# Performance work log

Measured on AMD Instinct MI355X. Metric: run time of the kernel, lower is better.

The kernel has to match this reference:

```python
import jax, jax.numpy as jnp
import numpy as np

HEADS = 4
DIM_HEAD = 64
SCALE = DIM_HEAD ** -0.5


def setup_inputs() -> dict:
    key = jax.random.key(0)
    k1, k2, k3 = jax.random.split(key, 3)
    C = 256
    hidden = HEADS * DIM_HEAD  # 256
    x = jax.random.normal(k1, (16, C, 64, 64), dtype=jnp.float32)
    # 1x1 conv weights collapsed to [out, in] matrices
    w_qkv = jax.random.normal(k2, (3 * hidden, C), dtype=jnp.float32) * (C ** -0.5)
    w_out = jax.random.normal(k3, (C, hidden), dtype=jnp.float32) * (hidden ** -0.5)
    b_out = jnp.zeros((C,), dtype=jnp.float32)
    return {"x": x, "w_qkv": w_qkv, "w_out": w_out, "b_out": b_out}


def reference(x, w_qkv, w_out, b_out):
    b, c, h, w = x.shape
    n = h * w
    # 1x1 conv == channel GEMM
    qkv = jnp.einsum('bchw,oc->bohw', x, w_qkv)           # [b, 3*hidden, h, w]
    qkv = qkv.reshape(b, 3, HEADS, DIM_HEAD, n)            # [b, 3, H, d, n]
    q, k, v = qkv[:, 0], qkv[:, 1], qkv[:, 2]              # each [b, H, d, n]
    q = jax.nn.softmax(q, axis=2) * SCALE                  # softmax over d
    k = jax.nn.softmax(k, axis=3)                          # softmax over n
    context = jnp.einsum('bhdn,bhen->bhde', k, v)          # [b, H, d, e]
    out = jnp.einsum('bhde,bhdn->bhen', context, q)        # [b, H, e, n]
    out = out.reshape(b, HEADS * DIM_HEAD, h, w)           # [b, hidden, h, w]
    return jnp.einsum('bchw,oc->bohw', out, w_out) + b_out[None, :, None, None]
```

## Files before the change

kernel.cpp:

```cpp
#include <hip/hip_runtime.h>

#define NPIX 4096
#define SCALE 0.125f

typedef _Float16 half8 __attribute__((ext_vector_type(8)));
typedef _Float16 half4 __attribute__((ext_vector_type(4)));
typedef float floatx4 __attribute__((ext_vector_type(4)));

__device__ __forceinline__ void async16(void* lds, const void* g) {
  __builtin_amdgcn_global_load_lds(
      (const __attribute__((address_space(1))) unsigned int*)(uintptr_t)g,
      (__attribute__((address_space(3))) unsigned int*)(unsigned)(uintptr_t)lds,
      16, 0, 0);
}

__global__ __launch_bounds__(256) void split16_kernel(const float* __restrict__ w,
                                                      _Float16* __restrict__ hi,
                                                      _Float16* __restrict__ lo, int n) {
  int i = blockIdx.x * 256 + threadIdx.x;
  if (i < n) {
    float v = w[i];
    _Float16 h = (_Float16)v;
    hi[i] = h;
    lo[i] = (_Float16)(v - (float)h);
  }
}

__global__ __launch_bounds__(256) void transpose16_kernel(const float* __restrict__ x,
                                                          _Float16* __restrict__ xt) {
  __shared__ float t[64][65];
  const int n0 = blockIdx.x * 64, c0 = blockIdx.y * 64, b = blockIdx.z;
  const float* xp = x + (long)b * 256 * NPIX;
  const int tid = threadIdx.x;
  const int r = tid >> 4, c4 = (tid & 15) * 4;
#pragma unroll
  for (int p = 0; p < 4; p++) {
    float4 v = *(const float4*)&xp[(long)(c0 + r + p * 16) * NPIX + n0 + c4];
    t[r + p * 16][c4 + 0] = v.x;
    t[r + p * 16][c4 + 1] = v.y;
    t[r + p * 16][c4 + 2] = v.z;
    t[r + p * 16][c4 + 3] = v.w;
  }
  __syncthreads();
  const int n = tid >> 2, cg = (tid & 3) * 16;
  alignas(16) _Float16 o[16];
#pragma unroll
  for (int i = 0; i < 16; i++) o[i] = (_Float16)t[cg + i][n];
  _Float16* dst = &xt[((long)b * NPIX + n0 + n) * 256 + c0 + cg];
  *(float4*)dst = *(float4*)&o[0];
  *(float4*)(dst + 8) = *(float4*)&o[8];
}

__global__ __launch_bounds__(256) void q_gemm_softmax(const _Float16* __restrict__ Ahp,
                                                      const _Float16* __restrict__ Alp,
                                                      const _Float16* __restrict__ Bt,
                                                      _Float16* __restrict__ PT) {
  union alignas(16) QU {
    _Float16 st[2][3][128 * 32];
    _Float16 pt[128][128];
  };
  __shared__ QU u;
  const int tid = threadIdx.x;
  const int n0 = blockIdx.x * 128, m0 = blockIdx.y * 128;
  const int bz = blockIdx.z;
  const _Float16* Bp = Bt + (long)bz * NPIX * 256;
  const int wv = tid >> 6, l = tid & 63;
  const int r16 = l & 15, q = l >> 4;
  const int mb = (wv >> 1) * 64, nb = (wv & 1) * 64;
  const int r1 = tid >> 2;
  const int o1 = ((tid & 3) * 8) ^ (((r1 >> 1) & 3) * 8);
  const int r2 = r1 + 64;
  const int ldsc1 = (wv * 64) * 8;
  const int ldsc2 = (256 + wv * 64) * 8;
  const int q8 = (q * 8) ^ (((r16 >> 1) & 3) * 8);

  auto STAGE = [&](int buf, int kt) {
    const int k0 = kt * 32;
    async16(&u.st[buf][0][ldsc1], &Ahp[(long)(m0 + r1) * 256 + k0 + o1]);
    async16(&u.st[buf][0][ldsc2], &Ahp[(long)(m0 + r2) * 256 + k0 + o1]);
    async16(&u.st[buf][1][ldsc1], &Alp[(long)(m0 + r1) * 256 + k0 + o1]);
    async16(&u.st[buf][1][ldsc2], &Alp[(long)(m0 + r2) * 256 + k0 + o1]);
    async16(&u.st[buf][2][ldsc1], &Bp[(long)(n0 + r1) * 256 + k0 + o1]);
    async16(&u.st[buf][2][ldsc2], &Bp[(long)(n0 + r2) * 256 + k0 + o1]);
  };

  floatx4 acc[4][4];
#pragma unroll
  for (int i = 0; i < 4; i++)
#pragma unroll
    for (int j = 0; j < 4; j++) acc[i][j] = (floatx4){0.f, 0.f, 0.f, 0.f};

  STAGE(0, 0);
  __syncthreads();
  int cur = 0;
  for (int kt = 0; kt < 8; kt++) {
    if (kt < 7) STAGE(cur ^ 1, kt + 1);
    half8 fa[4], flo[4], fb[4];
#pragma unroll
    for (int i = 0; i < 4; i++) {
      fa[i] = *(const half8*)&u.st[cur][0][(mb + i * 16 + r16) * 32 + q8];
      flo[i] = *(const half8*)&u.st[cur][1][(mb + i * 16 + r16) * 32 + q8];
      fb[i] = *(const half8*)&u.st[cur][2][(nb + i * 16 + r16) * 32 + q8];
    }
#pragma unroll
    for (int i = 0; i < 4; i++)
#pragma unroll
      for (int j = 0; j < 4; j++) {
        acc[i][j] = __builtin_amdgcn_mfma_f32_16x16x32_f16(fa[i], fb[j], acc[i][j], 0, 0, 0);
        acc[i][j] = __builtin_amdgcn_mfma_f32_16x16x32_f16(flo[i], fb[j], acc[i][j], 0, 0, 0);
      }
    __syncthreads();
    cur ^= 1;
  }

#pragma unroll
  for (int j = 0; j < 4; j++) {
    float s = 0.f;
#pragma unroll
    for (int i = 0; i < 4; i++)
#pragma unroll
      for (int t = 0; t < 4; t++) {
        float e = __expf(acc[i][j][t]);
        acc[i][j][t] = e;
        s += e;
      }
    s += __shfl_xor(s, 16, 64);
    s += __shfl_xor(s, 32, 64);
    const float rinv = 1.0f / s;
    const int nl = nb + j * 16 + r16;
    const int swz = (nl & 7) * 8;
#pragma unroll
    for (int i = 0; i < 4; i++) {
      half4 h4;
#pragma unroll
      for (int t = 0; t < 4; t++) h4[t] = (_Float16)(acc[i][j][t] * rinv);
      *(half4*)&u.pt[nl][(mb + i * 16 + q * 4) ^ swz] = h4;
    }
  }
  __syncthreads();
  const int rbase = tid >> 4, c16 = tid & 15;
  _Float16* dst = PT + ((long)(bz * 2 + (m0 >> 7)) * NPIX + n0) * 128;
#pragma unroll
  for (int k = 0; k < 8; k++) {
    const int row = rbase + k * 16;
    const int chunk = c16 ^ (row & 7);
    float4 v = *(const float4*)&u.pt[row][chunk * 8];
    *(float4*)&dst[(long)row * 128 + c16 * 8] = v;
  }
}

#define CPB 2
__global__ __launch_bounds__(256) void kv_ctx_gemm(const _Float16* __restrict__ Ahp,
                                                   const _Float16* __restrict__ Bt,
                                                   float* __restrict__ pbuf,
                                                   float* __restrict__ rsbuf) {
  union alignas(16) KVU {
    _Float16 st[2][2][128 * 32];
    _Float16 ev[128][136];
  };
  __shared__ KVU u;
  const int tid = threadIdx.x;
  const int cg = blockIdx.x;
  const int hi = blockIdx.y;
  const int b = blockIdx.z;
  const _Float16* Bp = Bt + (long)b * NPIX * 256;
  const int wv = tid >> 6, l = tid & 63;
  const int r16 = l & 15, q = l >> 4;
  const int mb = (wv >> 1) * 64, nb = (wv & 1) * 64;
  const int r1 = tid >> 2;
  const int o1 = ((tid & 3) * 8) ^ (((r1 >> 1) & 3) * 8);
  const int ldsc1 = (wv * 64) * 8;
  const int ldsc2 = (256 + wv * 64) * 8;
  const int q8 = (q * 8) ^ (((r16 >> 1) & 3) * 8);
  const long gAk = (long)(256 + hi * 64 + r1) * 256;
  const long gAv = (long)(512 + hi * 64 + r1) * 256;

  auto STAGE = [&](int buf, int kt, int n0) {
    const int k0 = kt * 32;
    async16(&u.st[buf][0][ldsc1], &Ahp[gAk + k0 + o1]);
    async16(&u.st[buf][0][ldsc2], &Ahp[gAv + k0 + o1]);
    async16(&u.st[buf][1][ldsc1], &Bp[(long)(n0 + r1) * 256 + k0 + o1]);
    async16(&u.st[buf][1][ldsc2], &Bp[(long)(n0 + 64 + r1) * 256 + k0 + o1]);
  };

  floatx4 c2[4];
#pragma unroll
  for (int j = 0; j < 4; j++) c2[j] = (floatx4){0.f, 0.f, 0.f, 0.f};
  float rs = 0.f;

  for (int cs = 0; cs < CPB; cs++) {
    const int n0 = (cg * CPB + cs) * 128;
    floatx4 acc[4][4];
#pragma unroll
    for (int i = 0; i < 4; i++)
#pragma unroll
      for (int j = 0; j < 4; j++) acc[i][j] = (floatx4){0.f, 0.f, 0.f, 0.f};

    STAGE(0, 0, n0);
    __syncthreads();
    int cur = 0;
    for (int kt = 0; kt < 8; kt++) {
      if (kt < 7) STAGE(cur ^ 1, kt + 1, n0);
      half8 fa[4], fb[4];
#pragma unroll
      for (int i = 0; i < 4; i++) {
        fa[i] = *(const half8*)&u.st[cur][0][(mb + i * 16 + r16) * 32 + q8];
        fb[i] = *(const half8*)&u.st[cur][1][(nb + i * 16 + r16) * 32 + q8];
      }
#pragma unroll
      for (int i = 0; i < 4; i++)
#pragma unroll
        for (int j = 0; j < 4; j++) {
          acc[i][j] = __builtin_amdgcn_mfma_f32_16x16x32_f16(fa[i], fb[j], acc[i][j], 0, 0, 0);
        }
      __syncthreads();
      cur ^= 1;
    }

    const bool is_k = (mb == 0);
#pragma unroll
    for (int i = 0; i < 4; i++) {
      const int row = mb + i * 16 + q * 4;
#pragma unroll
      for (int j = 0; j < 4; j++) {
        const int col = nb + j * 16 + r16;
#pragma unroll
        for (int t = 0; t < 4; t++) {
          const float vv0 = acc[i][j][t];
          u.ev[row + t][col] = (_Float16)(is_k ? __expf(vv0) : vv0);
        }
      }
    }
    __syncthreads();

#pragma unroll
    for (int ks = 0; ks < 4; ks++) {
      half8 a = *(const half8*)&u.ev[wv * 16 + r16][ks * 32 + q * 8];
#pragma unroll
      for (int ii = 0; ii < 8; ii++) rs += (float)a[ii];
#pragma unroll
      for (int j = 0; j < 4; j++) {
        half8 bv = *(const half8*)&u.ev[64 + j * 16 + r16][ks * 32 + q * 8];
        c2[j] = __builtin_amdgcn_mfma_f32_16x16x32_f16(a, bv, c2[j], 0, 0, 0);
      }
    }
    __syncthreads();
  }

  rs += __shfl_xor(rs, 16, 64);
  rs += __shfl_xor(rs, 32, 64);
  const int bh = b * 4 + hi;
  float* pp = pbuf + ((long)bh * 16 + cg) * 4096;
#pragma unroll
  for (int j = 0; j < 4; j++)
#pragma unroll
    for (int reg = 0; reg < 4; reg++)
      pp[(wv * 16 + q * 4 + reg) * 64 + j * 16 + r16] = c2[j][reg];
  if (l < 16) rsbuf[((long)bh * 16 + cg) * 64 + wv * 16 + r16] = rs;
}

__global__ __launch_bounds__(256) void mctx_fused(const float* __restrict__ w_out,
                                                  const float* __restrict__ pbuf,
                                                  const float* __restrict__ rsbuf,
                                                  _Float16* __restrict__ Mhi,
                                                  _Float16* __restrict__ Mlo) {
  __shared__ float sctxT[64][65];
  __shared__ float sinv[64];
  const int cq = blockIdx.x, h = blockIdx.y, b = blockIdx.z;
  const int bh = b * 4 + h;
  const float* pp = pbuf + (long)bh * 16 * 4096;
  const int tid = threadIdx.x;
  {
    const int d = tid >> 2, e0 = (tid & 3) * 16;
    float s0[16];
#pragma unroll
    for (int i = 0; i < 16; i++) s0[i] = 0.f;
    for (int c = 0; c < 16; c++) {
#pragma unroll
      for (int k = 0; k < 4; k++) {
        float4 v = *(const float4*)&pp[(long)c * 4096 + d * 64 + e0 + k * 4];
        s0[k * 4 + 0] += v.x;
        s0[k * 4 + 1] += v.y;
        s0[k * 4 + 2] += v.z;
        s0[k * 4 + 3] += v.w;
      }
    }
#pragma unroll
    for (int i = 0; i < 16; i++) sctxT[e0 + i][d] = s0[i];
  }
  if (tid < 64) {
    const float* rp = rsbuf + (long)bh * 16 * 64 + tid;
    float z = 0.f;
#pragma unroll
    for (int c = 0; c < 16; c++) z += rp[c * 64];
    sinv[tid] = 1.0f / z;
  }
  __syncthreads();
  const int c = cq * 64 + (tid >> 2);
  const int d0 = (tid & 3) * 16;
  const float* wp = w_out + (long)c * 256 + h * 64;
  float acc[16];
#pragma unroll
  for (int i = 0; i < 16; i++) acc[i] = 0.f;
#pragma unroll
  for (int e4 = 0; e4 < 16; e4++) {
    float4 wv = *(const float4*)&wp[e4 * 4];
#pragma unroll
    for (int u2 = 0; u2 < 4; u2++) {
      const float we = ((const float*)&wv)[u2];
      const int e = e4 * 4 + u2;
#pragma unroll
      for (int dd = 0; dd < 16; dd++) acc[dd] = fmaf(we, sctxT[e][d0 + dd], acc[dd]);
    }
  }
  alignas(16) _Float16 hi16[16], lo16[16];
#pragma unroll
  for (int k4 = 0; k4 < 4; k4++) {
    float4 zv = *(const float4*)&sinv[d0 + k4 * 4];
#pragma unroll
    for (int u2 = 0; u2 < 4; u2++) {
      const int dd = k4 * 4 + u2;
      float v = acc[dd] * (SCALE * ((const float*)&zv)[u2]);
      _Float16 hh = (_Float16)v;
      hi16[dd] = hh;
      lo16[dd] = (_Float16)(v - (float)hh);
    }
  }
  _Float16* mh = Mhi + ((long)b * 256 + c) * 256 + h * 64 + d0;
  _Float16* ml = Mlo + ((long)b * 256 + c) * 256 + h * 64 + d0;
#pragma unroll
  for (int k = 0; k < 2; k++) {
    *(float4*)&mh[k * 8] = *(float4*)&hi16[k * 8];
    *(float4*)&ml[k * 8] = *(float4*)&lo16[k * 8];
  }
}

__global__ __launch_bounds__(256) void out_gemm(const _Float16* __restrict__ Mhi,
                                                const _Float16* __restrict__ Mlo,
                                                const _Float16* __restrict__ PT,
                                                float* __restrict__ C,
                                                const float* __restrict__ bias) {
  __shared__ _Float16 st[2][3][128 * 32];
  const int tid = threadIdx.x;
  const int n0 = blockIdx.x * 128, m0 = blockIdx.y * 128;
  const int b = blockIdx.z;
  const _Float16* Ah = Mhi + (long)b * 65536;
  const _Float16* Al = Mlo + (long)b * 65536;
  float* Cp = C + (long)b * 256 * NPIX;
  const int wv = tid >> 6, l = tid & 63;
  const int r16 = l & 15, q = l >> 4;
  const int mb = (wv >> 1) * 64, nb = (wv & 1) * 64;
  const int r1 = tid >> 2;
  const int o1 = ((tid & 3) * 8) ^ (((r1 >> 1) & 3) * 8);
  const int r2 = r1 + 64;
  const int ldsc1 = (wv * 64) * 8;
  const int ldsc2 = (256 + wv * 64) * 8;
  const int q8 = (q * 8) ^ (((r16 >> 1) & 3) * 8);

  auto STAGE = [&](int buf, int kt) {
    const int k0 = kt * 32;
    async16(&st[buf][0][ldsc1], &Ah[(long)(m0 + r1) * 256 + k0 + o1]);
    async16(&st[buf][0][ldsc2], &Ah[(long)(m0 + r2) * 256 + k0 + o1]);
    async16(&st[buf][1][ldsc1], &Al[(long)(m0 + r1) * 256 + k0 + o1]);
    async16(&st[buf][1][ldsc2], &Al[(long)(m0 + r2) * 256 + k0 + o1]);
    const _Float16* Bk = PT + ((long)(b * 2 + (kt >> 2)) * NPIX + n0) * 128;
    async16(&st[buf][2][ldsc1], &Bk[(long)r1 * 128 + (kt & 3) * 32 + o1]);
    async16(&st[buf][2][ldsc2], &Bk[(long)(r1 + 64) * 128 + (kt & 3) * 32 + o1]);
  };

  floatx4 acc[4][4];
#pragma unroll
  for (int i = 0; i < 4; i++)
#pragma unroll
    for (int j = 0; j < 4; j++) acc[i][j] = (floatx4){0.f, 0.f, 0.f, 0.f};

  STAGE(0, 0);
  __syncthreads();
  int cur = 0;
  for (int kt = 0; kt < 8; kt++) {
    if (kt < 7) STAGE(cur ^ 1, kt + 1);
    half8 fa[4], flo[4], fb[4];
#pragma unroll
    for (int i = 0; i < 4; i++) {
      fa[i] = *(const half8*)&st[cur][0][(mb + i * 16 + r16) * 32 + q8];
      flo[i] = *(const half8*)&st[cur][1][(mb + i * 16 + r16) * 32 + q8];
      fb[i] = *(const half8*)&st[cur][2][(nb + i * 16 + r16) * 32 + q8];
    }
#pragma unroll
    for (int i = 0; i < 4; i++)
#pragma unroll
      for (int j = 0; j < 4; j++) {
        acc[i][j] = __builtin_amdgcn_mfma_f32_16x16x32_f16(fa[i], fb[j], acc[i][j], 0, 0, 0);
        acc[i][j] = __builtin_amdgcn_mfma_f32_16x16x32_f16(flo[i], fb[j], acc[i][j], 0, 0, 0);
      }
    __syncthreads();
    cur ^= 1;
  }
#pragma unroll
  for (int i = 0; i < 4; i++) {
    const int mrow = m0 + mb + i * 16 + q * 4;
#pragma unroll
    for (int t = 0; t < 4; t++) {
      float bz = bias[mrow + t];
#pragma unroll
      for (int j = 0; j < 4; j++) {
        Cp[(long)(mrow + t) * NPIX + n0 + nb + j * 16 + r16] = acc[i][j][t] + bz;
      }
    }
  }
}

extern "C" void kernel_launch(void* const* d_in, const int* in_sizes, int n_in,
                              void* d_out, int out_size, void* d_ws, size_t ws_size,
                              hipStream_t stream) {
  const float* x = (const float*)d_in[0];
  const float* w_qkv = (const float*)d_in[1];
  const float* w_out = (const float*)d_in[2];
  const float* b_out = (const float*)d_in[3];
  float* out = (float*)d_out;

  _Float16* PT = (_Float16*)d_ws;
  float* rsbuf = (float*)(PT + (long)16 * 2 * NPIX * 128);
  _Float16* wq_hi = (_Float16*)(rsbuf + 64 * 16 * 64);
  _Float16* wq_lo = wq_hi + 768 * 256;
  _Float16* Mhi = wq_lo + 768 * 256;
  _Float16* Mlo = Mhi + 16 * 256 * 256;
  _Float16* xt = (_Float16*)d_out;
  float* pbuf = (float*)d_out + (1 << 23);

  split16_kernel<<<768, 256, 0, stream>>>(w_qkv, wq_hi, wq_lo, 768 * 256);
  transpose16_kernel<<<dim3(64, 4, 16), 256, 0, stream>>>(x, xt);
  kv_ctx_gemm<<<dim3(16, 4, 16), 256, 0, stream>>>(wq_hi, xt, pbuf, rsbuf);
  mctx_fused<<<dim3(4, 4, 16), 256, 0, stream>>>(w_out, pbuf, rsbuf, Mhi, Mlo);
  q_gemm_softmax<<<dim3(32, 2, 16), 256, 0, stream>>>(wq_hi, wq_lo, xt, PT);
  out_gemm<<<dim3(32, 2, 16), 256, 0, stream>>>(Mhi, Mlo, PT, out, b_out);
}
```

Before: 208.4 us.

## Merge weight split with transpose and interleave Q and KV GEMMs in one launch

```diff
diff --git a/kernel.cpp b/kernel.cpp
--- a/kernel.cpp
+++ b/kernel.cpp
@@ -14,24 +14,27 @@
       16, 0, 0);
 }
 
-__global__ __launch_bounds__(256) void split16_kernel(const float* __restrict__ w,
-                                                      _Float16* __restrict__ hi,
-                                                      _Float16* __restrict__ lo, int n) {
-  int i = blockIdx.x * 256 + threadIdx.x;
-  if (i < n) {
-    float v = w[i];
-    _Float16 h = (_Float16)v;
-    hi[i] = h;
-    lo[i] = (_Float16)(v - (float)h);
-  }
-}
-
-__global__ __launch_bounds__(256) void transpose16_kernel(const float* __restrict__ x,
-                                                          _Float16* __restrict__ xt) {
+__global__ __launch_bounds__(256) void prep_kernel(const float* __restrict__ x,
+                                                   _Float16* __restrict__ xt,
+                                                   const float* __restrict__ w_qkv,
+                                                   _Float16* __restrict__ wq_hi,
+                                                   _Float16* __restrict__ wq_lo) {
+  const int tid = threadIdx.x;
+  if (blockIdx.z == 16) {
+    int base = (blockIdx.x * 4 + blockIdx.y) * 256 + tid;
+#pragma unroll
+    for (int r = 0; r < 3; r++) {
+      int i = base + r * 65536;
+      float v = w_qkv[i];
+      _Float16 h = (_Float16)v;
+      wq_hi[i] = h;
+      wq_lo[i] = (_Float16)(v - (float)h);
+    }
+    return;
+  }
   __shared__ float t[64][65];
   const int n0 = blockIdx.x * 64, c0 = blockIdx.y * 64, b = blockIdx.z;
   const float* xp = x + (long)b * 256 * NPIX;
-  const int tid = threadIdx.x;
   const int r = tid >> 4, c4 = (tid & 15) * 4;
 #pragma unroll
   for (int p = 0; p < 4; p++) {
@@ -51,18 +54,21 @@
   *(float4*)(dst + 8) = *(float4*)&o[8];
 }
 
-__global__ __launch_bounds__(256) void q_gemm_softmax(const _Float16* __restrict__ Ahp,
-                                                      const _Float16* __restrict__ Alp,
-                                                      const _Float16* __restrict__ Bt,
-                                                      _Float16* __restrict__ PT) {
-  union alignas(16) QU {
-    _Float16 st[2][3][128 * 32];
-    _Float16 pt[128][128];
-  };
-  __shared__ QU u;
+union alignas(16) MU {
+  _Float16 q_st[2][3][128 * 32];
+  _Float16 q_pt[128][128];
+  _Float16 k_st[2][2][128 * 32];
+  _Float16 k_ev[128][136];
+};
+
+__device__ __forceinline__ void q_body(MU& u, int idx,
+                                       const _Float16* __restrict__ Ahp,
+                                       const _Float16* __restrict__ Alp,
+                                       const _Float16* __restrict__ Bt,
+                                       _Float16* __restrict__ PT) {
   const int tid = threadIdx.x;
-  const int n0 = blockIdx.x * 128, m0 = blockIdx.y * 128;
-  const int bz = blockIdx.z;
+  const int n0 = (idx & 31) * 128, m0 = ((idx >> 5) & 1) * 128;
+  const int bz = idx >> 6;
   const _Float16* Bp = Bt + (long)bz * NPIX * 256;
   const int wv = tid >> 6, l = tid & 63;
   const int r16 = l & 15, q = l >> 4;
@@ -76,12 +82,12 @@
 
   auto STAGE = [&](int buf, int kt) {
     const int k0 = kt * 32;
-    async16(&u.st[buf][0][ldsc1], &Ahp[(long)(m0 + r1) * 256 + k0 + o1]);
-    async16(&u.st[buf][0][ldsc2], &Ahp[(long)(m0 + r2) * 256 + k0 + o1]);
-    async16(&u.st[buf][1][ldsc1], &Alp[(long)(m0 + r1) * 256 + k0 + o1]);
-    async16(&u.st[buf][1][ldsc2], &Alp[(long)(m0 + r2) * 256 + k0 + o1]);
-    async16(&u.st[buf][2][ldsc1], &Bp[(long)(n0 + r1) * 256 + k0 + o1]);
-    async16(&u.st[buf][2][ldsc2], &Bp[(long)(n0 + r2) * 256 + k0 + o1]);
+    async16(&u.q_st[buf][0][ldsc1], &Ahp[(long)(m0 + r1) * 256 + k0 + o1]);
+    async16(&u.q_st[buf][0][ldsc2], &Ahp[(long)(m0 + r2) * 256 + k0 + o1]);
+    async16(&u.q_st[buf][1][ldsc1], &Alp[(long)(m0 + r1) * 256 + k0 + o1]);
+    async16(&u.q_st[buf][1][ldsc2], &Alp[(long)(m0 + r2) * 256 + k0 + o1]);
+    async16(&u.q_st[buf][2][ldsc1], &Bp[(long)(n0 + r1) * 256 + k0 + o1]);
+    async16(&u.q_st[buf][2][ldsc2], &Bp[(long)(n0 + r2) * 256 + k0 + o1]);
   };
 
   floatx4 acc[4][4];
@@ -98,9 +104,9 @@
     half8 fa[4], flo[4], fb[4];
 #pragma unroll
     for (int i = 0; i < 4; i++) {
-      fa[i] = *(const half8*)&u.st[cur][0][(mb + i * 16 + r16) * 32 + q8];
-      flo[i] = *(const half8*)&u.st[cur][1][(mb + i * 16 + r16) * 32 + q8];
-      fb[i] = *(const half8*)&u.st[cur][2][(nb + i * 16 + r16) * 32 + q8];
+      fa[i] = *(const half8*)&u.q_st[cur][0][(mb + i * 16 + r16) * 32 + q8];
+      flo[i] = *(const half8*)&u.q_st[cur][1][(mb + i * 16 + r16) * 32 + q8];
+      fb[i] = *(const half8*)&u.q_st[cur][2][(nb + i * 16 + r16) * 32 + q8];
     }
 #pragma unroll
     for (int i = 0; i < 4; i++)
@@ -134,7 +140,7 @@
       half4 h4;
 #pragma unroll
       for (int t = 0; t < 4; t++) h4[t] = (_Float16)(acc[i][j][t] * rinv);
-      *(half4*)&u.pt[nl][(mb + i * 16 + q * 4) ^ swz] = h4;
+      *(half4*)&u.q_pt[nl][(mb + i * 16 + q * 4) ^ swz] = h4;
     }
   }
   __syncthreads();
@@ -144,25 +150,20 @@
   for (int k = 0; k < 8; k++) {
     const int row = rbase + k * 16;
     const int chunk = c16 ^ (row & 7);
-    float4 v = *(const float4*)&u.pt[row][chunk * 8];
+    float4 v = *(const float4*)&u.q_pt[row][chunk * 8];
     *(float4*)&dst[(long)row * 128 + c16 * 8] = v;
   }
 }
 
-#define CPB 2
-__global__ __launch_bounds__(256) void kv_ctx_gemm(const _Float16* __restrict__ Ahp,
-                                                   const _Float16* __restrict__ Bt,
-                                                   float* __restrict__ pbuf,
-                                                   float* __restrict__ rsbuf) {
-  union alignas(16) KVU {
-    _Float16 st[2][2][128 * 32];
-    _Float16 ev[128][136];
-  };
-  __shared__ KVU u;
+__device__ __forceinline__ void kv_body(MU& u, int idx,
+                                        const _Float16* __restrict__ Ahp,
+                                        const _Float16* __restrict__ Bt,
+                                        float* __restrict__ pbuf,
+                                        float* __restrict__ rsbuf) {
   const int tid = threadIdx.x;
-  const int cg = blockIdx.x;
-  const int hi = blockIdx.y;
-  const int b = blockIdx.z;
+  const int cg = idx & 15;
+  const int hi = (idx >> 4) & 3;
+  const int b = idx >> 6;
   const _Float16* Bp = Bt + (long)b * NPIX * 256;
   const int wv = tid >> 6, l = tid & 63;
   const int r16 = l & 15, q = l >> 4;
@@ -177,10 +178,10 @@
 
   auto STAGE = [&](int buf, int kt, int n0) {
     const int k0 = kt * 32;
-    async16(&u.st[buf][0][ldsc1], &Ahp[gAk + k0 + o1]);
-    async16(&u.st[buf][0][ldsc2], &Ahp[gAv + k0 + o1]);
-    async16(&u.st[buf][1][ldsc1], &Bp[(long)(n0 + r1) * 256 + k0 + o1]);
-    async16(&u.st[buf][1][ldsc2], &Bp[(long)(n0 + 64 + r1) * 256 + k0 + o1]);
+    async16(&u.k_st[buf][0][ldsc1], &Ahp[gAk + k0 + o1]);
+    async16(&u.k_st[buf][0][ldsc2], &Ahp[gAv + k0 + o1]);
+    async16(&u.k_st[buf][1][ldsc1], &Bp[(long)(n0 + r1) * 256 + k0 + o1]);
+    async16(&u.k_st[buf][1][ldsc2], &Bp[(long)(n0 + 64 + r1) * 256 + k0 + o1]);
   };
 
   floatx4 c2[4];
@@ -188,8 +189,8 @@
   for (int j = 0; j < 4; j++) c2[j] = (floatx4){0.f, 0.f, 0.f, 0.f};
   float rs = 0.f;
 
-  for (int cs = 0; cs < CPB; cs++) {
-    const int n0 = (cg * CPB + cs) * 128;
+  for (int cs = 0; cs < 2; cs++) {
+    const int n0 = (cg * 2 + cs) * 128;
     floatx4 acc[4][4];
 #pragma unroll
     for (int i = 0; i < 4; i++)
@@ -204,15 +205,14 @@
       half8 fa[4], fb[4];
 #pragma unroll
       for (int i = 0; i < 4; i++) {
-        fa[i] = *(const half8*)&u.st[cur][0][(mb + i * 16 + r16) * 32 + q8];
-        fb[i] = *(const half8*)&u.st[cur][1][(nb + i * 16 + r16) * 32 + q8];
+        fa[i] = *(const half8*)&u.k_st[cur][0][(mb + i * 16 + r16) * 32 + q8];
+        fb[i] = *(const half8*)&u.k_st[cur][1][(nb + i * 16 + r16) * 32 + q8];
       }
 #pragma unroll
       for (int i = 0; i < 4; i++)
 #pragma unroll
-        for (int j = 0; j < 4; j++) {
+        for (int j = 0; j < 4; j++)
           acc[i][j] = __builtin_amdgcn_mfma_f32_16x16x32_f16(fa[i], fb[j], acc[i][j], 0, 0, 0);
-        }
       __syncthreads();
       cur ^= 1;
     }
@@ -227,7 +227,7 @@
 #pragma unroll
         for (int t = 0; t < 4; t++) {
           const float vv0 = acc[i][j][t];
-          u.ev[row + t][col] = (_Float16)(is_k ? __expf(vv0) : vv0);
+          u.k_ev[row + t][col] = (_Float16)(is_k ? __expf(vv0) : vv0);
         }
       }
     }
@@ -235,12 +235,12 @@
 
 #pragma unroll
     for (int ks = 0; ks < 4; ks++) {
-      half8 a = *(const half8*)&u.ev[wv * 16 + r16][ks * 32 + q * 8];
+      half8 a = *(const half8*)&u.k_ev[wv * 16 + r16][ks * 32 + q * 8];
 #pragma unroll
       for (int ii = 0; ii < 8; ii++) rs += (float)a[ii];
 #pragma unroll
       for (int j = 0; j < 4; j++) {
-        half8 bv = *(const half8*)&u.ev[64 + j * 16 + r16][ks * 32 + q * 8];
+        half8 bv = *(const half8*)&u.k_ev[64 + j * 16 + r16][ks * 32 + q * 8];
         c2[j] = __builtin_amdgcn_mfma_f32_16x16x32_f16(a, bv, c2[j], 0, 0, 0);
       }
     }
@@ -257,6 +257,20 @@
     for (int reg = 0; reg < 4; reg++)
       pp[(wv * 16 + q * 4 + reg) * 64 + j * 16 + r16] = c2[j][reg];
   if (l < 16) rsbuf[((long)bh * 16 + cg) * 64 + wv * 16 + r16] = rs;
+}
+
+__global__ __launch_bounds__(256) void qkv_mega(const _Float16* __restrict__ wq_hi,
+                                                const _Float16* __restrict__ wq_lo,
+                                                const _Float16* __restrict__ xt,
+                                                _Float16* __restrict__ PT,
+                                                float* __restrict__ pbuf,
+                                                float* __restrict__ rsbuf) {
+  __shared__ MU u;
+  const int idx = blockIdx.x >> 1;
+  if ((blockIdx.x & 1) == 0)
+    q_body(u, idx, wq_hi, wq_lo, xt, PT);
+  else
+    kv_body(u, idx, wq_hi, xt, pbuf, rsbuf);
 }
 
 __global__ __launch_bounds__(256) void mctx_fused(const float* __restrict__ w_out,
@@ -428,10 +442,8 @@
   _Float16* xt = (_Float16*)d_out;
   float* pbuf = (float*)d_out + (1 << 23);
 
-  split16_kernel<<<768, 256, 0, stream>>>(w_qkv, wq_hi, wq_lo, 768 * 256);
-  transpose16_kernel<<<dim3(64, 4, 16), 256, 0, stream>>>(x, xt);
-  kv_ctx_gemm<<<dim3(16, 4, 16), 256, 0, stream>>>(wq_hi, xt, pbuf, rsbuf);
+  prep_kernel<<<dim3(64, 4, 17), 256, 0, stream>>>(x, xt, w_qkv, wq_hi, wq_lo);
+  qkv_mega<<<2048, 256, 0, stream>>>(wq_hi, wq_lo, xt, PT, pbuf, rsbuf);
   mctx_fused<<<dim3(4, 4, 16), 256, 0, stream>>>(w_out, pbuf, rsbuf, Mhi, Mlo);
-  q_gemm_softmax<<<dim3(32, 2, 16), 256, 0, stream>>>(wq_hi, wq_lo, xt, PT);
   out_gemm<<<dim3(32, 2, 16), 256, 0, stream>>>(Mhi, Mlo, PT, out, b_out);
 }
```

Measured after the change: 213.0 us. 1.02x slower.

## Triple-buffer LDS staging with partial vmcnt waits in GEMM kernels

Applied to the files above, without the earlier changes.

```diff
diff --git a/kernel.cpp b/kernel.cpp
--- a/kernel.cpp
+++ b/kernel.cpp
@@ -12,6 +12,19 @@
       (const __attribute__((address_space(1))) unsigned int*)(uintptr_t)g,
       (__attribute__((address_space(3))) unsigned int*)(unsigned)(uintptr_t)lds,
       16, 0, 0);
+}
+
+__device__ __forceinline__ void vmwait(int n) {
+  if (n >= 6)      asm volatile("s_waitcnt vmcnt(6)" ::: "memory");
+  else if (n >= 4) asm volatile("s_waitcnt vmcnt(4)" ::: "memory");
+  else             asm volatile("s_waitcnt vmcnt(0)" ::: "memory");
+}
+
+__device__ __forceinline__ void pipe_barrier(int n) {
+  __builtin_amdgcn_sched_barrier(0);
+  vmwait(n);
+  __builtin_amdgcn_s_barrier();
+  __builtin_amdgcn_sched_barrier(0);
 }
 
 __global__ __launch_bounds__(256) void split16_kernel(const float* __restrict__ w,
@@ -56,7 +69,7 @@
                                                       const _Float16* __restrict__ Bt,
                                                       _Float16* __restrict__ PT) {
   union alignas(16) QU {
-    _Float16 st[2][3][128 * 32];
+    _Float16 st[3][3][128 * 32];
     _Float16 pt[128][128];
   };
   __shared__ QU u;
@@ -91,16 +104,21 @@
     for (int j = 0; j < 4; j++) acc[i][j] = (floatx4){0.f, 0.f, 0.f, 0.f};
 
   STAGE(0, 0);
-  __syncthreads();
-  int cur = 0;
+  STAGE(1, 1);
+  pipe_barrier(6);
+  int cc = 0;
   for (int kt = 0; kt < 8; kt++) {
-    if (kt < 7) STAGE(cur ^ 1, kt + 1);
+    if (kt < 6) {
+      int sb = cc + 2;
+      if (sb >= 3) sb -= 3;
+      STAGE(sb, kt + 2);
+    }
     half8 fa[4], flo[4], fb[4];
 #pragma unroll
     for (int i = 0; i < 4; i++) {
-      fa[i] = *(const half8*)&u.st[cur][0][(mb + i * 16 + r16) * 32 + q8];
-      flo[i] = *(const half8*)&u.st[cur][1][(mb + i * 16 + r16) * 32 + q8];
-      fb[i] = *(const half8*)&u.st[cur][2][(nb + i * 16 + r16) * 32 + q8];
+      fa[i] = *(const half8*)&u.st[cc][0][(mb + i * 16 + r16) * 32 + q8];
+      flo[i] = *(const half8*)&u.st[cc][1][(mb + i * 16 + r16) * 32 + q8];
+      fb[i] = *(const half8*)&u.st[cc][2][(nb + i * 16 + r16) * 32 + q8];
     }
 #pragma unroll
     for (int i = 0; i < 4; i++)
@@ -109,8 +127,8 @@
         acc[i][j] = __builtin_amdgcn_mfma_f32_16x16x32_f16(fa[i], fb[j], acc[i][j], 0, 0, 0);
         acc[i][j] = __builtin_amdgcn_mfma_f32_16x16x32_f16(flo[i], fb[j], acc[i][j], 0, 0, 0);
       }
-    __syncthreads();
-    cur ^= 1;
+    pipe_barrier(kt < 6 ? 6 : 0);
+    cc = (cc == 2) ? 0 : cc + 1;
   }
 
 #pragma unroll
@@ -155,7 +173,7 @@
                                                    float* __restrict__ pbuf,
                                                    float* __restrict__ rsbuf) {
   union alignas(16) KVU {
-    _Float16 st[2][2][128 * 32];
+    _Float16 st[3][2][128 * 32];
     _Float16 ev[128][136];
   };
   __shared__ KVU u;
@@ -197,24 +215,28 @@
       for (int j = 0; j < 4; j++) acc[i][j] = (floatx4){0.f, 0.f, 0.f, 0.f};
 
     STAGE(0, 0, n0);
-    __syncthreads();
-    int cur = 0;
+    STAGE(1, 1, n0);
+    pipe_barrier(4);
+    int cc = 0;
     for (int kt = 0; kt < 8; kt++) {
-      if (kt < 7) STAGE(cur ^ 1, kt + 1, n0);
+      if (kt < 6) {
+        int sb = cc + 2;
+        if (sb >= 3) sb -= 3;
+        STAGE(sb, kt + 2, n0);
+      }
       half8 fa[4], fb[4];
 #pragma unroll
       for (int i = 0; i < 4; i++) {
-        fa[i] = *(const half8*)&u.st[cur][0][(mb + i * 16 + r16) * 32 + q8];
-        fb[i] = *(const half8*)&u.st[cur][1][(nb + i * 16 + r16) * 32 + q8];
+        fa[i] = *(const half8*)&u.st[cc][0][(mb + i * 16 + r16) * 32 + q8];
+        fb[i] = *(const half8*)&u.st[cc][1][(nb + i * 16 + r16) * 32 + q8];
       }
 #pragma unroll
       for (int i = 0; i < 4; i++)
 #pragma unroll
-        for (int j = 0; j < 4; j++) {
+        for (int j = 0; j < 4; j++)
           acc[i][j] = __builtin_amdgcn_mfma_f32_16x16x32_f16(fa[i], fb[j], acc[i][j], 0, 0, 0);
-        }
-      __syncthreads();
-      cur ^= 1;
+      pipe_barrier(kt < 6 ? 4 : 0);
+      cc = (cc == 2) ? 0 : cc + 1;
     }
 
     const bool is_k = (mb == 0);
@@ -340,7 +362,7 @@
                                                 const _Float16* __restrict__ PT,
                                                 float* __restrict__ C,
                                                 const float* __restrict__ bias) {
-  __shared__ _Float16 st[2][3][128 * 32];
+  __shared__ _Float16 st[3][3][128 * 32];
   const int tid = threadIdx.x;
   const int n0 = blockIdx.x * 128, m0 = blockIdx.y * 128;
   const int b = blockIdx.z;
@@ -375,16 +397,21 @@
     for (int j = 0; j < 4; j++) acc[i][j] = (floatx4){0.f, 0.f, 0.f, 0.f};
 
   STAGE(0, 0);
-  __syncthreads();
-  int cur = 0;
+  STAGE(1, 1);
+  pipe_barrier(6);
+  int cc = 0;
   for (int kt = 0; kt < 8; kt++) {
-    if (kt < 7) STAGE(cur ^ 1, kt + 1);
+    if (kt < 6) {
+      int sb = cc + 2;
+      if (sb >= 3) sb -= 3;
+      STAGE(sb, kt + 2);
+    }
     half8 fa[4], flo[4], fb[4];
 #pragma unroll
     for (int i = 0; i < 4; i++) {
-      fa[i] = *(const half8*)&st[cur][0][(mb + i * 16 + r16) * 32 + q8];
-      flo[i] = *(const half8*)&st[cur][1][(mb + i * 16 + r16) * 32 + q8];
-      fb[i] = *(const half8*)&st[cur][2][(nb + i * 16 + r16) * 32 + q8];
+      fa[i] = *(const half8*)&st[cc][0][(mb + i * 16 + r16) * 32 + q8];
+      flo[i] = *(const half8*)&st[cc][1][(mb + i * 16 + r16) * 32 + q8];
+      fb[i] = *(const half8*)&st[cc][2][(nb + i * 16 + r16) * 32 + q8];
     }
 #pragma unroll
     for (int i = 0; i < 4; i++)
@@ -393,8 +420,8 @@
         acc[i][j] = __builtin_amdgcn_mfma_f32_16x16x32_f16(fa[i], fb[j], acc[i][j], 0, 0, 0);
         acc[i][j] = __builtin_amdgcn_mfma_f32_16x16x32_f16(flo[i], fb[j], acc[i][j], 0, 0, 0);
       }
-    __syncthreads();
-    cur ^= 1;
+    pipe_barrier(kt < 6 ? 6 : 0);
+    cc = (cc == 2) ? 0 : cc + 1;
   }
 #pragma unroll
   for (int i = 0; i < 4; i++) {
```

Result: no change. 209.6 us (+0.6%).
